# Kernel tuning notes

Measured on AMD Instinct MI355X. Metric: run time of the kernel, lower is better.

Reference implementation:

```python
import jax, jax.numpy as jnp
import numpy as np

NUM_HEADS = 16
HEAD_DIM = 64
ROPE_THETA = 10000.0


def _rope_cos_sin(n, dtype):
    # Llama RoPE: inv_freq over even dims, emb = concat(freqs, freqs)
    inv_freq = 1.0 / (ROPE_THETA ** (jnp.arange(0, HEAD_DIM, 2, dtype=jnp.float32) / HEAD_DIM))
    freqs = jnp.arange(n, dtype=jnp.float32)[:, None] * inv_freq[None, :]  # [N, D/2]
    emb = jnp.concatenate([freqs, freqs], axis=-1)  # [N, D]
    return jnp.cos(emb).astype(dtype), jnp.sin(emb).astype(dtype)


def _rotate_half(x):
    x1, x2 = jnp.split(x, 2, axis=-1)
    return jnp.concatenate([-x2, x1], axis=-1)


def setup_inputs() -> dict:
    key = jax.random.key(0)
    ks = jax.random.split(key, 5)
    B, N, H = 2, 2048, 1024
    feature = jax.random.normal(ks[0], (B, N, H), dtype=jnp.float32)
    attention_mask = jnp.ones((B, N), dtype=jnp.int32)
    scale = 0.02
    Wq = jax.random.normal(ks[1], (H, H), dtype=jnp.float32) * scale
    Wk = jax.random.normal(ks[2], (H, H), dtype=jnp.float32) * scale
    Wv = jax.random.normal(ks[3], (H, H), dtype=jnp.float32) * scale
    Wo = jax.random.normal(ks[4], (H, H), dtype=jnp.float32) * scale
    return {"feature": feature, "attention_mask": attention_mask,
            "Wq": Wq, "Wk": Wk, "Wv": Wv, "Wo": Wo}


def reference(feature, attention_mask, Wq, Wk, Wv, Wo):
    B, N, H = feature.shape
    h, d = NUM_HEADS, HEAD_DIM
    scale = d ** -0.5

    def proj(x, W):  # nn.Linear(bias=False): x @ W.T
        y = jnp.einsum('bnh,oh->bno', x, W)
        return y.reshape(B, N, h, d).transpose(0, 2, 1, 3)  # [B,h,N,d]

    q, k, v = proj(feature, Wq), proj(feature, Wk), proj(feature, Wv)

    cos, sin = _rope_cos_sin(N, feature.dtype)  # [N, d]
    cos = cos[None, None]  # [1,1,N,d]
    sin = sin[None, None]
    q = q * cos + _rotate_half(q) * sin
    k = k * cos + _rotate_half(k) * sin

    scores = jnp.einsum('bhqd,bhkd->bhqk', q, k) * scale  # [B,h,N,N]
    mask = (attention_mask != 0)[:, None, None, :]  # [B,1,1,N]
    scores = jnp.where(mask, scores, jnp.float32(-jnp.inf).astype(scores.dtype))
    weights = jax.nn.softmax(scores, axis=-1)

    out = jnp.einsum('bhqk,bhkd->bhqd', weights, v)  # [B,h,N,d]
    out = out.transpose(0, 2, 1, 3).reshape(B, N, H)
    return jnp.einsum('bnh,oh->bno', out, Wo)
```

## Files before the change

kernel.cpp:

```cpp
#include <hip/hip_runtime.h>
#include <hip/hip_bf16.h>

typedef __attribute__((ext_vector_type(4))) float f32x4;
typedef __attribute__((ext_vector_type(8))) short s16x8;
typedef __attribute__((ext_vector_type(4))) short s16x4;

#define BB 2
#define NN 2048
#define HH 1024
#define NHEAD 16
#define HDIM 64

__device__ __forceinline__ short f2bf(float f) {
  union { float f; unsigned u; } v; v.f = f;
  unsigned r = v.u + 0x7fffu + ((v.u >> 16) & 1u);
  return (short)(r >> 16);
}

__device__ __forceinline__ f32x4 zf4() { f32x4 z; z[0]=0.f; z[1]=0.f; z[2]=0.f; z[3]=0.f; return z; }

__device__ __forceinline__ f32x4 mfma16(s16x8 a, s16x8 b, f32x4 c) {
  return __builtin_amdgcn_mfma_f32_16x16x32_bf16(a, b, c, 0, 0, 0);
}

__device__ __forceinline__ s16x4 cvt4(f32x4 v) {
  s16x4 o; o[0]=f2bf(v[0]); o[1]=f2bf(v[1]); o[2]=f2bf(v[2]); o[3]=f2bf(v[3]); return o;
}

__device__ __forceinline__ float vexp2(float x) {
  float r; asm("v_exp_f32 %0, %1" : "=v"(r) : "v"(x)); return r;
}

__device__ __forceinline__ float vrcp(float x) {
  float r; asm("v_rcp_f32 %0, %1" : "=v"(r) : "v"(x)); return r;
}

__device__ __forceinline__ unsigned cvtpk_bf16(float lo, float hi) {
  unsigned r; asm("v_cvt_pk_bf16_f32 %0, %1, %2" : "=v"(r) : "v"(lo), "v"(hi)); return r;
}

__device__ __forceinline__ void gload_lds16(const short* g, short* l) {
  __builtin_amdgcn_global_load_lds(
      (const __attribute__((address_space(1))) unsigned*)g,
      (__attribute__((address_space(3))) unsigned*)l, 16, 0, 0);
}

__global__ __launch_bounds__(256) void prep_kernel(
    const float* __restrict__ feat, const int* __restrict__ mask,
    const float* __restrict__ wq, const float* __restrict__ wk,
    const float* __restrict__ wv, const float* __restrict__ wo,
    short* __restrict__ fbf, short* __restrict__ wqb, short* __restrict__ wkb,
    short* __restrict__ wvb, short* __restrict__ wob,
    float* __restrict__ cosb, float* __restrict__ sinb,
    float* __restrict__ mbias, int* __restrict__ mseg) {
  const int tid = blockIdx.x * blockDim.x + threadIdx.x;
  const int nth = gridDim.x * blockDim.x;
  const int NF4 = BB*NN*HH/4;
  for (int i = tid; i < NF4; i += nth)
    ((s16x4*)fbf)[i] = cvt4(((const f32x4*)feat)[i]);
  const int NW4 = HH*HH/4;
  for (int i = tid; i < NW4; i += nth) {
    ((s16x4*)wqb)[i] = cvt4(((const f32x4*)wq)[i]);
    ((s16x4*)wkb)[i] = cvt4(((const f32x4*)wk)[i]);
    ((s16x4*)wvb)[i] = cvt4(((const f32x4*)wv)[i]);
    ((s16x4*)wob)[i] = cvt4(((const f32x4*)wo)[i]);
  }
  for (int i = tid; i < NN*32; i += nth) {
    int pos = i >> 5, f = i & 31;
    float inv = __expf(-(float)f * 0.28782313662425572f);
    float ang = (float)pos * inv;
    float s, c;
    sincosf(ang, &s, &c);
    cosb[i] = c; sinb[i] = s;
  }
  for (int i = tid; i < BB*NN; i += nth)
    mbias[i] = mask[i] ? 0.f : -1.0e30f;
  for (int i = tid; i < BB*(NN/64); i += nth) {
    int bb = i / (NN/64), sg = i % (NN/64);
    int any = 0;
    for (int j = 0; j < 64; ++j) any |= (mask[bb*NN + sg*64 + j] == 0);
    mseg[i] = any;
  }
}

__device__ __forceinline__ void gemm128_core(
    const short* __restrict__ A, const short* __restrict__ W,
    int bm, int bn, short* smem, f32x4 acc[4][4]) {
  const int tid = threadIdx.x;
  const int lane = tid & 63, wid = tid >> 6;
  const int wr = wid >> 1, wc = wid & 1;
  const int g = lane >> 4, lr = lane & 15;
#pragma unroll
  for (int i = 0; i < 4; ++i)
#pragma unroll
    for (int j = 0; j < 4; ++j) acc[i][j] = zf4();

  const int srow = wid*16 + (lane >> 2);
  const int scol = (lane & 3) * 8;
  const short* Abase = A + (size_t)(bm*128 + srow)*HH + scol;
  const short* Wbase = W + (size_t)(bn*128 + srow)*HH + scol;

  auto stage = [&](int b, int t) {
    const short* ga = Abase + t*32;
    const short* gb = Wbase + t*32;
    short* la = smem + b*8192 + wid*512;
    short* lb = smem + b*8192 + 4096 + wid*512;
    gload_lds16(ga,          la);
    gload_lds16(ga + 64*HH,  la + 2048);
    gload_lds16(gb,          lb);
    gload_lds16(gb + 64*HH,  lb + 2048);
  };

  stage(0, 0);
  asm volatile("s_waitcnt vmcnt(0)");
  __syncthreads();

  const int NT = HH / 32;
  int cur = 0;
  for (int t = 0; t < NT; ++t) {
    if (t + 1 < NT) stage(cur ^ 1, t + 1);
    const short* At = smem + cur*8192;
    const short* Bt = At + 4096;
    s16x8 af[4], bf[4];
#pragma unroll
    for (int mf = 0; mf < 4; ++mf)
      af[mf] = *(const s16x8*)&At[(wr*64 + mf*16 + lr)*32 + g*8];
#pragma unroll
    for (int nf = 0; nf < 4; ++nf)
      bf[nf] = *(const s16x8*)&Bt[(wc*64 + nf*16 + lr)*32 + g*8];
#pragma unroll
    for (int mf = 0; mf < 4; ++mf)
#pragma unroll
      for (int nf = 0; nf < 4; ++nf)
        acc[mf][nf] = mfma16(af[mf], bf[nf], acc[mf][nf]);
    __syncthreads();
    cur ^= 1;
  }
}

__global__ __launch_bounds__(256) void qkv_kernel(
    const short* __restrict__ fbf, const short* __restrict__ wqb,
    const short* __restrict__ wkb, const short* __restrict__ wvb,
    const float* __restrict__ cosb, const float* __restrict__ sinb,
    short* __restrict__ qb, short* __restrict__ kb, short* __restrict__ vtb) {
  __shared__ short smem[18432];
  const int bm = blockIdx.y, bn = blockIdx.x, z = blockIdx.z;
  const short* W = (z == 0) ? wqb : ((z == 1) ? wkb : wvb);
  f32x4 acc[4][4];
  gemm128_core(fbf, W, bm, bn, smem, acc);

  const int tid = threadIdx.x, lane = tid & 63, wid = tid >> 6;
  const int wr = wid >> 1, wc = wid & 1, g = lane >> 4, lr = lane & 15;
  const int head = bn*2 + wc;
  const int m0 = bm*128 + wr*64;
  const int b = m0 / NN;

  if (z < 2) {
    short* dst = (z == 0) ? qb : kb;
    const float scale = (z == 0) ? 0.18033688011112042f : 1.0f;
#pragma unroll
    for (int mf = 0; mf < 4; ++mf) {
#pragma unroll
      for (int r = 0; r < 4; ++r) {
        int m = m0 + mf*16 + g*4 + r;
        int n = m & (NN - 1);
        float c0 = cosb[n*32 + lr],      s0 = sinb[n*32 + lr];
        float c1 = cosb[n*32 + 16 + lr], s1 = sinb[n*32 + 16 + lr];
        float v0 = acc[mf][0][r], v1 = acc[mf][1][r];
        float v2 = acc[mf][2][r], v3 = acc[mf][3][r];
        float o0 = (v0*c0 - v2*s0) * scale;
        float o1 = (v1*c1 - v3*s1) * scale;
        float o2 = (v2*c0 + v0*s0) * scale;
        float o3 = (v3*c1 + v1*s1) * scale;
        size_t base = ((size_t)(b*NHEAD + head)*NN + n)*HDIM;
        dst[base +  0 + lr] = f2bf(o0);
        dst[base + 16 + lr] = f2bf(o1);
        dst[base + 32 + lr] = f2bf(o2);
        dst[base + 48 + lr] = f2bf(o3);
      }
    }
  } else {
    __syncthreads();
    short* tp = smem + wid*4608;
#pragma unroll
    for (int mf = 0; mf < 4; ++mf)
#pragma unroll
      for (int nf = 0; nf < 4; ++nf)
#pragma unroll
        for (int r = 0; r < 4; ++r)
          tp[(nf*16 + lr)*72 + mf*16 + g*4 + r] = f2bf(acc[mf][nf][r]);
    __syncthreads();
    const int nbase = m0 & (NN - 1);
    size_t vbase = ((size_t)(b*NHEAD + head)*HDIM)*NN;
#pragma unroll
    for (int it = 0; it < 8; ++it) {
      int j  = it*8 + (lane >> 3);
      int ns = (lane & 7)*8;
      s16x8 vv = *(const s16x8*)&tp[j*72 + ns];
      *(s16x8*)&vtb[vbase + (size_t)j*NN + nbase + ns] = vv;
    }
  }
}

__global__ __launch_bounds__(256) void attn_kernel(
    const short* __restrict__ qb, const short* __restrict__ kb,
    const short* __restrict__ vtb, const float* __restrict__ mbias,
    const int* __restrict__ mseg,
    short* __restrict__ attnb) {
  __shared__ short Kt[64*72];
  __shared__ short Vt[64*72];
  __shared__ __align__(16) unsigned Pd[4][16*36];
  const int tid = threadIdx.x, lane = tid & 63, wid = tid >> 6;
  const int g = lane >> 4, lr = lane & 15;
  const int bh = blockIdx.y; const int b = bh >> 4;
  const int q0 = blockIdx.x*64 + wid*16;

  const short* qp = qb + ((size_t)bh*NN + q0 + lr)*HDIM + g*8;
  s16x8 qf0 = *(const s16x8*)(qp);
  s16x8 qf1 = *(const s16x8*)(qp + 32);

  f32x4 acc[4];
#pragma unroll
  for (int i = 0; i < 4; ++i) acc[i] = zf4();
  float mrun = -3.0e38f, lsum = 0.f;

  const int sr = tid >> 2;
  const int sc = (tid & 3) * 16;
  const short* kp = kb + (size_t)bh*NN*HDIM + (size_t)sr*HDIM + sc;
  const short* vp = vtb + ((size_t)bh*HDIM + sr)*NN + sc;
  const float* mb = mbias + b*NN;
  const int* msp = mseg + b*(NN/64);

  s16x8 kr0 = *(const s16x8*)(kp);
  s16x8 kr1 = *(const s16x8*)(kp + 8);
  s16x8 vr0 = *(const s16x8*)(vp);
  s16x8 vr1 = *(const s16x8*)(vp + 8);

  for (int k0 = 0; k0 < NN; k0 += 64) {
    *(s16x8*)&Kt[sr*72 + sc]     = kr0;
    *(s16x8*)&Kt[sr*72 + sc + 8] = kr1;
    *(s16x8*)&Vt[sr*72 + sc]     = vr0;
    *(s16x8*)&Vt[sr*72 + sc + 8] = vr1;
    __syncthreads();
    if (k0 + 64 < NN) {
      kp += 64*HDIM; vp += 64;
      kr0 = *(const s16x8*)(kp);
      kr1 = *(const s16x8*)(kp + 8);
      vr0 = *(const s16x8*)(vp);
      vr1 = *(const s16x8*)(vp + 8);
    }

    f32x4 s[4];
    __builtin_amdgcn_s_setprio(1);
#pragma unroll
    for (int kg = 0; kg < 4; ++kg) {
      s16x8 ka0 = *(const s16x8*)&Kt[(kg*16 + lr)*72 + g*8];
      s16x8 ka1 = *(const s16x8*)&Kt[(kg*16 + lr)*72 + 32 + g*8];
      s[kg] = mfma16(ka1, qf1, mfma16(ka0, qf0, zf4()));
    }
    __builtin_amdgcn_s_setprio(0);

    if (msp[k0 >> 6]) {
#pragma unroll
      for (int kg = 0; kg < 4; ++kg) {
        f32x4 bi = *(const f32x4*)&mb[k0 + kg*16 + g*4];
#pragma unroll
        for (int r = 0; r < 4; ++r) s[kg][r] += bi[r];
      }
    }

    float m0a = fmaxf(fmaxf(s[0][0], s[0][1]), fmaxf(s[0][2], s[0][3]));
    float m1a = fmaxf(fmaxf(s[1][0], s[1][1]), fmaxf(s[1][2], s[1][3]));
    float m2a = fmaxf(fmaxf(s[2][0], s[2][1]), fmaxf(s[2][2], s[2][3]));
    float m3a = fmaxf(fmaxf(s[3][0], s[3][1]), fmaxf(s[3][2], s[3][3]));
    float rmax = fmaxf(fmaxf(m0a, m1a), fmaxf(m2a, m3a));
    rmax = fmaxf(rmax, __shfl_xor(rmax, 16));
    rmax = fmaxf(rmax, __shfl_xor(rmax, 32));

    if (__any(rmax > mrun + 8.f)) {
      float mnew = fmaxf(mrun, rmax);
      float al = vexp2(mrun - mnew);
      mrun = mnew;
      lsum *= al;
      float alr[4];
#pragma unroll
      for (int r = 0; r < 4; ++r)
        alr[r] = __shfl(al, (lane & 48) | (g*4 + r));
#pragma unroll
      for (int db = 0; db < 4; ++db)
#pragma unroll
        for (int r = 0; r < 4; ++r) acc[db][r] *= alr[r];
    }

#pragma unroll
    for (int kg = 0; kg < 4; ++kg) {
      float p0 = vexp2(s[kg][0] - mrun);
      float p1 = vexp2(s[kg][1] - mrun);
      float p2 = vexp2(s[kg][2] - mrun);
      float p3 = vexp2(s[kg][3] - mrun);
      lsum += (p0 + p1) + (p2 + p3);
      unsigned* prow = &Pd[wid][lr*36 + kg*8 + g*2];
      prow[0] = cvtpk_bf16(p0, p1);
      prow[1] = cvtpk_bf16(p2, p3);
    }

    s16x8 pa0 = *(const s16x8*)&Pd[wid][lr*36 + g*4];
    s16x8 pa1 = *(const s16x8*)&Pd[wid][lr*36 + 16 + g*4];
    __builtin_amdgcn_s_setprio(1);
#pragma unroll
    for (int db = 0; db < 4; ++db) {
      s16x8 vb0 = *(const s16x8*)&Vt[(db*16 + lr)*72 + g*8];
      s16x8 vb1 = *(const s16x8*)&Vt[(db*16 + lr)*72 + 32 + g*8];
      acc[db] = mfma16(pa0, vb0, acc[db]);
      acc[db] = mfma16(pa1, vb1, acc[db]);
    }
    __builtin_amdgcn_s_setprio(0);
    __syncthreads();
  }

  lsum += __shfl_xor(lsum, 16);
  lsum += __shfl_xor(lsum, 32);
  float inv = vrcp(lsum);
  float invr[4];
#pragma unroll
  for (int r = 0; r < 4; ++r)
    invr[r] = __shfl(inv, (lane & 48) | (g*4 + r));
#pragma unroll
  for (int r = 0; r < 4; ++r) {
    size_t row = (size_t)(b*NN + q0 + g*4 + r);
#pragma unroll
    for (int db = 0; db < 4; ++db)
      attnb[row*HH + (bh & 15)*64 + db*16 + lr] = f2bf(acc[db][r]*invr[r]);
  }
}

__global__ __launch_bounds__(256) void outproj_kernel(
    const short* __restrict__ attnb, const short* __restrict__ wob,
    float* __restrict__ out) {
  __shared__ short smem[16384];
  const int bm = blockIdx.y, bn = blockIdx.x;
  f32x4 acc[4][4];
  gemm128_core(attnb, wob, bm, bn, smem, acc);
  const int tid = threadIdx.x, lane = tid & 63, wid = tid >> 6;
  const int wr = wid >> 1, wc = wid & 1, g = lane >> 4, lr = lane & 15;
  const int m0 = bm*128 + wr*64;
  const int c0 = bn*128 + wc*64;
#pragma unroll
  for (int mf = 0; mf < 4; ++mf)
#pragma unroll
    for (int r = 0; r < 4; ++r) {
      int m = m0 + mf*16 + g*4 + r;
      float* po = out + (size_t)m*HH + c0;
#pragma unroll
      for (int nf = 0; nf < 4; ++nf)
        po[nf*16 + lr] = acc[mf][nf][r];
    }
}

extern "C" void kernel_launch(void* const* d_in, const int* in_sizes, int n_in,
                              void* d_out, int out_size, void* d_ws, size_t ws_size,
                              hipStream_t stream) {
  const float* feat = (const float*)d_in[0];
  const int*   mask = (const int*)d_in[1];
  const float* wq   = (const float*)d_in[2];
  const float* wk   = (const float*)d_in[3];
  const float* wv   = (const float*)d_in[4];
  const float* wo   = (const float*)d_in[5];
  float* out = (float*)d_out;

  char* ws = (char*)d_ws;
  size_t off = 0;
  short* fbf = (short*)(ws + off); off += (size_t)BB*NN*HH*2;
  short* wqb = (short*)(ws + off); off += (size_t)HH*HH*2;
  short* wkb = (short*)(ws + off); off += (size_t)HH*HH*2;
  short* wvb = (short*)(ws + off); off += (size_t)HH*HH*2;
  short* wob = (short*)(ws + off); off += (size_t)HH*HH*2;
  float* cosb = (float*)(ws + off); off += (size_t)NN*32*4;
  float* sinb = (float*)(ws + off); off += (size_t)NN*32*4;
  float* mbias = (float*)(ws + off); off += (size_t)BB*NN*4;
  int* msegb = (int*)(ws + off); off += (size_t)BB*(NN/64)*4;
  short* qbuf = (short*)(ws + off); off += (size_t)BB*NN*HH*2;
  short* kbuf = (short*)(ws + off); off += (size_t)BB*NN*HH*2;
  short* vtbuf = (short*)(ws + off); off += (size_t)BB*NN*HH*2;
  short* attnb = (short*)(ws + off); off += (size_t)BB*NN*HH*2;

  prep_kernel<<<1024, 256, 0, stream>>>(feat, mask, wq, wk, wv, wo,
                                        fbf, wqb, wkb, wvb, wob, cosb, sinb,
                                        mbias, msegb);
  qkv_kernel<<<dim3(HH/128, BB*NN/128, 3), 256, 0, stream>>>(
      fbf, wqb, wkb, wvb, cosb, sinb, qbuf, kbuf, vtbuf);
  attn_kernel<<<dim3(NN/64, BB*NHEAD), 256, 0, stream>>>(
      qbuf, kbuf, vtbuf, mbias, msegb, attnb);
  outproj_kernel<<<dim3(HH/128, BB*NN/128), 256, 0, stream>>>(attnb, wob, out);
}
```

Baseline: 134.6 us.

## Double-buffer K/V in LDS and keep softmax P in registers via permuted K rows

The attention kernel now double-buffers K and V tiles in LDS, so each iteration needs one barrier instead of two. K rows are stored in a permuted order so the score MFMA output layout matches the A-operand layout of the PV MFMA, which removes the Pd LDS round-trip for probabilities. The row sum is computed by an extra MFMA against a ones vector, replacing the shuffle reductions, and the row max uses v_max3. The cost is double the K/V LDS footprint and two extra MFMAs per tile. The bias indexing is remapped to follow the permuted key order.

```diff
diff --git a/kernel.cpp b/kernel.cpp
--- a/kernel.cpp
+++ b/kernel.cpp
@@ -33,6 +33,10 @@
 
 __device__ __forceinline__ float vrcp(float x) {
   float r; asm("v_rcp_f32 %0, %1" : "=v"(r) : "v"(x)); return r;
+}
+
+__device__ __forceinline__ float vmax3(float a, float b, float c) {
+  float r; asm("v_max3_f32 %0, %1, %2, %3" : "=v"(r) : "v"(a), "v"(b), "v"(c)); return r;
 }
 
 __device__ __forceinline__ unsigned cvtpk_bf16(float lo, float hi) {
@@ -207,9 +211,8 @@
     const short* __restrict__ vtb, const float* __restrict__ mbias,
     const int* __restrict__ mseg,
     short* __restrict__ attnb) {
-  __shared__ short Kt[64*72];
-  __shared__ short Vt[64*72];
-  __shared__ __align__(16) unsigned Pd[4][16*36];
+  __shared__ short Kt[2][64*72];
+  __shared__ short Vt[2][64*72];
   const int tid = threadIdx.x, lane = tid & 63, wid = tid >> 6;
   const int g = lane >> 4, lr = lane & 15;
   const int bh = blockIdx.y; const int b = bh >> 4;
@@ -219,13 +222,19 @@
   s16x8 qf0 = *(const s16x8*)(qp);
   s16x8 qf1 = *(const s16x8*)(qp + 32);
 
+  s16x8 one8;
+#pragma unroll
+  for (int i = 0; i < 8; ++i) one8[i] = (short)0x3F80;
+
   f32x4 acc[4];
 #pragma unroll
   for (int i = 0; i < 4; ++i) acc[i] = zf4();
-  float mrun = -3.0e38f, lsum = 0.f;
+  f32x4 accl = zf4();
+  float mrun = -3.0e38f;
 
   const int sr = tid >> 2;
   const int sc = (tid & 3) * 16;
+  const int rK = ((sr >> 5) & 1)*32 + ((sr >> 2) & 1)*16 + ((sr >> 3) & 3)*4 + (sr & 3);
   const short* kp = kb + (size_t)bh*NN*HDIM + (size_t)sr*HDIM + sc;
   const short* vp = vtb + ((size_t)bh*HDIM + sr)*NN + sc;
   const float* mb = mbias + b*NN;
@@ -235,45 +244,50 @@
   s16x8 kr1 = *(const s16x8*)(kp + 8);
   s16x8 vr0 = *(const s16x8*)(vp);
   s16x8 vr1 = *(const s16x8*)(vp + 8);
-
+  *(s16x8*)&Kt[0][rK*72 + sc]     = kr0;
+  *(s16x8*)&Kt[0][rK*72 + sc + 8] = kr1;
+  *(s16x8*)&Vt[0][sr*72 + sc]     = vr0;
+  *(s16x8*)&Vt[0][sr*72 + sc + 8] = vr1;
+  __syncthreads();
+
+  int cur = 0;
   for (int k0 = 0; k0 < NN; k0 += 64) {
-    *(s16x8*)&Kt[sr*72 + sc]     = kr0;
-    *(s16x8*)&Kt[sr*72 + sc + 8] = kr1;
-    *(s16x8*)&Vt[sr*72 + sc]     = vr0;
-    *(s16x8*)&Vt[sr*72 + sc + 8] = vr1;
-    __syncthreads();
-    if (k0 + 64 < NN) {
+    const bool nl = (k0 + 64 < NN);
+    if (nl) {
       kp += 64*HDIM; vp += 64;
       kr0 = *(const s16x8*)(kp);
       kr1 = *(const s16x8*)(kp + 8);
       vr0 = *(const s16x8*)(vp);
       vr1 = *(const s16x8*)(vp + 8);
     }
+    const short* KtC = Kt[cur];
+    const short* VtC = Vt[cur];
 
     f32x4 s[4];
     __builtin_amdgcn_s_setprio(1);
 #pragma unroll
-    for (int kg = 0; kg < 4; ++kg) {
-      s16x8 ka0 = *(const s16x8*)&Kt[(kg*16 + lr)*72 + g*8];
-      s16x8 ka1 = *(const s16x8*)&Kt[(kg*16 + lr)*72 + 32 + g*8];
-      s[kg] = mfma16(ka1, qf1, mfma16(ka0, qf0, zf4()));
+    for (int j = 0; j < 4; ++j) {
+      s16x8 ka0 = *(const s16x8*)&KtC[(j*16 + lr)*72 + g*8];
+      s16x8 ka1 = *(const s16x8*)&KtC[(j*16 + lr)*72 + 32 + g*8];
+      s[j] = mfma16(ka1, qf1, mfma16(ka0, qf0, zf4()));
     }
     __builtin_amdgcn_s_setprio(0);
 
     if (msp[k0 >> 6]) {
 #pragma unroll
-      for (int kg = 0; kg < 4; ++kg) {
-        f32x4 bi = *(const f32x4*)&mb[k0 + kg*16 + g*4];
-#pragma unroll
-        for (int r = 0; r < 4; ++r) s[kg][r] += bi[r];
+      for (int j = 0; j < 4; ++j) {
+        f32x4 bi = *(const f32x4*)&mb[k0 + (j >> 1)*32 + (j & 1)*4 + g*8];
+#pragma unroll
+        for (int r = 0; r < 4; ++r) s[j][r] += bi[r];
       }
     }
 
-    float m0a = fmaxf(fmaxf(s[0][0], s[0][1]), fmaxf(s[0][2], s[0][3]));
-    float m1a = fmaxf(fmaxf(s[1][0], s[1][1]), fmaxf(s[1][2], s[1][3]));
-    float m2a = fmaxf(fmaxf(s[2][0], s[2][1]), fmaxf(s[2][2], s[2][3]));
-    float m3a = fmaxf(fmaxf(s[3][0], s[3][1]), fmaxf(s[3][2], s[3][3]));
-    float rmax = fmaxf(fmaxf(m0a, m1a), fmaxf(m2a, m3a));
+    float t0 = vmax3(s[0][0], s[0][1], s[0][2]);
+    float t1 = vmax3(s[0][3], s[1][0], s[1][1]);
+    float t2 = vmax3(s[1][2], s[1][3], s[2][0]);
+    float t3 = vmax3(s[2][1], s[2][2], s[2][3]);
+    float t4 = vmax3(s[3][0], s[3][1], s[3][2]);
+    float rmax = fmaxf(vmax3(t0, t1, t2), vmax3(t3, t4, s[3][3]));
     rmax = fmaxf(rmax, __shfl_xor(rmax, 16));
     rmax = fmaxf(rmax, __shfl_xor(rmax, 32));
 
@@ -281,56 +295,65 @@
       float mnew = fmaxf(mrun, rmax);
       float al = vexp2(mrun - mnew);
       mrun = mnew;
-      lsum *= al;
       float alr[4];
 #pragma unroll
       for (int r = 0; r < 4; ++r)
         alr[r] = __shfl(al, (lane & 48) | (g*4 + r));
 #pragma unroll
-      for (int db = 0; db < 4; ++db)
-#pragma unroll
-        for (int r = 0; r < 4; ++r) acc[db][r] *= alr[r];
-    }
-
-#pragma unroll
-    for (int kg = 0; kg < 4; ++kg) {
-      float p0 = vexp2(s[kg][0] - mrun);
-      float p1 = vexp2(s[kg][1] - mrun);
-      float p2 = vexp2(s[kg][2] - mrun);
-      float p3 = vexp2(s[kg][3] - mrun);
-      lsum += (p0 + p1) + (p2 + p3);
-      unsigned* prow = &Pd[wid][lr*36 + kg*8 + g*2];
-      prow[0] = cvtpk_bf16(p0, p1);
-      prow[1] = cvtpk_bf16(p2, p3);
-    }
-
-    s16x8 pa0 = *(const s16x8*)&Pd[wid][lr*36 + g*4];
-    s16x8 pa1 = *(const s16x8*)&Pd[wid][lr*36 + 16 + g*4];
+      for (int r = 0; r < 4; ++r) {
+        acc[0][r] *= alr[r]; acc[1][r] *= alr[r];
+        acc[2][r] *= alr[r]; acc[3][r] *= alr[r];
+        accl[r]   *= alr[r];
+      }
+    }
+
+    float p[4][4];
+#pragma unroll
+    for (int j = 0; j < 4; ++j) {
+      p[j][0] = vexp2(s[j][0] - mrun);
+      p[j][1] = vexp2(s[j][1] - mrun);
+      p[j][2] = vexp2(s[j][2] - mrun);
+      p[j][3] = vexp2(s[j][3] - mrun);
+    }
+    union { unsigned u[4]; s16x8 v; } A0, A1;
+    A0.u[0] = cvtpk_bf16(p[0][0], p[0][1]);
+    A0.u[1] = cvtpk_bf16(p[0][2], p[0][3]);
+    A0.u[2] = cvtpk_bf16(p[1][0], p[1][1]);
+    A0.u[3] = cvtpk_bf16(p[1][2], p[1][3]);
+    A1.u[0] = cvtpk_bf16(p[2][0], p[2][1]);
+    A1.u[1] = cvtpk_bf16(p[2][2], p[2][3]);
+    A1.u[2] = cvtpk_bf16(p[3][0], p[3][1]);
+    A1.u[3] = cvtpk_bf16(p[3][2], p[3][3]);
+
     __builtin_amdgcn_s_setprio(1);
+    accl = mfma16(A0.v, one8, accl);
+    accl = mfma16(A1.v, one8, accl);
 #pragma unroll
     for (int db = 0; db < 4; ++db) {
-      s16x8 vb0 = *(const s16x8*)&Vt[(db*16 + lr)*72 + g*8];
-      s16x8 vb1 = *(const s16x8*)&Vt[(db*16 + lr)*72 + 32 + g*8];
-      acc[db] = mfma16(pa0, vb0, acc[db]);
-      acc[db] = mfma16(pa1, vb1, acc[db]);
+      s16x8 vb0 = *(const s16x8*)&VtC[(db*16 + lr)*72 + g*8];
+      s16x8 vb1 = *(const s16x8*)&VtC[(db*16 + lr)*72 + 32 + g*8];
+      acc[db] = mfma16(A0.v, vb0, acc[db]);
+      acc[db] = mfma16(A1.v, vb1, acc[db]);
     }
     __builtin_amdgcn_s_setprio(0);
-    __syncthreads();
-  }
-
-  lsum += __shfl_xor(lsum, 16);
-  lsum += __shfl_xor(lsum, 32);
-  float inv = vrcp(lsum);
-  float invr[4];
-#pragma unroll
-  for (int r = 0; r < 4; ++r)
-    invr[r] = __shfl(inv, (lane & 48) | (g*4 + r));
+
+    if (nl) {
+      *(s16x8*)&Kt[cur^1][rK*72 + sc]     = kr0;
+      *(s16x8*)&Kt[cur^1][rK*72 + sc + 8] = kr1;
+      *(s16x8*)&Vt[cur^1][sr*72 + sc]     = vr0;
+      *(s16x8*)&Vt[cur^1][sr*72 + sc + 8] = vr1;
+      __syncthreads();
+      cur ^= 1;
+    }
+  }
+
 #pragma unroll
   for (int r = 0; r < 4; ++r) {
+    float inv = vrcp(accl[r]);
     size_t row = (size_t)(b*NN + q0 + g*4 + r);
 #pragma unroll
     for (int db = 0; db < 4; ++db)
-      attnb[row*HH + (bh & 15)*64 + db*16 + lr] = f2bf(acc[db][r]*invr[r]);
+      attnb[row*HH + (bh & 15)*64 + db*16 + lr] = f2bf(acc[db][r]*inv);
   }
 }
 
```

Result: faster. 130.2 us (-3.3%).
